# Kernel tuning notes

Hardware: AMD Instinct MI355X
Metric: run time of the kernel (lower is better)

The kernel has to match this reference:

```python
import jax, jax.numpy as jnp
import numpy as np

B, L, DIN, DQK = 16, 1024, 512, 128
NL, NC = 2, 2  # number of 'learnable' heads, number of 'cnn_projection' heads


def _conv1d(x_bcl, w, b):
    # x: [B, C_in, L], w: [C_out, C_in, 3], 'same' padding (kernel 3 -> pad 1)
    y = jax.lax.conv_general_dilated(x_bcl, w, (1,), [(1, 1)],
                                     dimension_numbers=('NCH', 'OIH', 'NCH'))
    return y + b[None, :, None]


def _attend(q, k, v, scale):
    # q,k,v: [H, B, L, D]; scale: [H]
    inv = 1.0 / jnp.sqrt(jnp.asarray(q.shape[-1], q.dtype))
    att = jax.nn.softmax(jnp.einsum('hbld,hbmd->hblm', q, k) * inv, axis=-1)
    out = scale[:, None, None, None] * jnp.einsum('hblm,hbmd->hbld', att, v)
    return out, att


def setup_inputs() -> dict:
    rk = jax.random.key(0)
    ks = jax.random.split(rk, 24)
    s = 0.02
    d = {}
    d['query'] = jax.random.normal(ks[0], (B, L, DIN), jnp.float32)
    d['key']   = jax.random.normal(ks[1], (B, L, DIN), jnp.float32)
    d['value'] = jax.random.normal(ks[2], (B, L, DIN), jnp.float32)
    # learnable (KQVProduct) heads: Linear dim_in -> dim_qk, stored as [in,out]
    d['lw_q'] = jax.random.normal(ks[3], (NL, DIN, DQK), jnp.float32) * s
    d['lb_q'] = jnp.zeros((NL, DQK), jnp.float32)
    d['lw_k'] = jax.random.normal(ks[4], (NL, DIN, DQK), jnp.float32) * s
    d['lb_k'] = jnp.zeros((NL, DQK), jnp.float32)
    d['lw_v'] = jax.random.normal(ks[5], (NL, DIN, DQK), jnp.float32) * s
    d['lb_v'] = jnp.zeros((NL, DQK), jnp.float32)
    d['lscale'] = jnp.ones((NL,), jnp.float32)
    # cnn_projection (KQVPCNN) heads: Conv1d(dim_in, dim_qk, k=3, pad=1)
    d['cw_q'] = jax.random.normal(ks[6], (NC, DQK, DIN, 3), jnp.float32) * s
    d['cb_q'] = jnp.zeros((NC, DQK), jnp.float32)
    d['cw_k'] = jax.random.normal(ks[7], (NC, DQK, DIN, 3), jnp.float32) * s
    d['cb_k'] = jnp.zeros((NC, DQK), jnp.float32)
    d['cw_v'] = jax.random.normal(ks[8], (NC, DQK, DIN, 3), jnp.float32) * s
    d['cb_v'] = jnp.zeros((NC, DQK), jnp.float32)
    d['cscale'] = jnp.ones((NC,), jnp.float32)
    # final projection: Linear((NL+NC)*dim_qk -> dim_in)
    d['proj_w'] = jax.random.normal(ks[9], ((NL + NC) * DQK, DIN), jnp.float32) * s
    d['proj_b'] = jnp.zeros((DIN,), jnp.float32)
    return d


def reference(query, key, value,
              lw_q, lb_q, lw_k, lb_k, lw_v, lb_v, lscale,
              cw_q, cb_q, cw_k, cb_k, cw_v, cb_v, cscale,
              proj_w, proj_b):
    # --- learnable heads (batched over head axis) ---
    lq = jnp.einsum('bld,hdk->hblk', query, lw_q) + lb_q[:, None, None, :]
    lk = jnp.einsum('bld,hdk->hblk', key,   lw_k) + lb_k[:, None, None, :]
    lv = jnp.einsum('bld,hdk->hblk', value, lw_v) + lb_v[:, None, None, :]
    lout, latt = _attend(lq, lk, lv, lscale)
    # --- cnn_projection heads ---
    qt = jnp.swapaxes(query, 1, 2)  # [B, DIN, L]
    kt = jnp.swapaxes(key, 1, 2)
    vt = jnp.swapaxes(value, 1, 2)
    cq = jnp.swapaxes(jax.vmap(lambda w, b: _conv1d(qt, w, b))(cw_q, cb_q), 2, 3)
    ck = jnp.swapaxes(jax.vmap(lambda w, b: _conv1d(kt, w, b))(cw_k, cb_k), 2, 3)
    cv = jnp.swapaxes(jax.vmap(lambda w, b: _conv1d(vt, w, b))(cw_v, cb_v), 2, 3)
    cout, catt = _attend(cq, ck, cv, cscale)  # [NC, B, L, DQK]
    # --- concat heads + final projection ---
    cat = jnp.concatenate([lout[0], lout[1], cout[0], cout[1]], axis=-1)  # [B,L,4*DQK]
    out = cat @ proj_w + proj_b
    return (out, latt[0], latt[1], catt[0], catt[1])
```

## Files before the change

kernel.cpp:

```cpp
#include <hip/hip_runtime.h>


using bf16_t = __bf16;
using bf16x8 = __attribute__((ext_vector_type(8))) __bf16;
using bf16x4 = __attribute__((ext_vector_type(4))) __bf16;
using f32x4  = __attribute__((ext_vector_type(4))) float;

#define NB   16
#define SL   1024
#define DIN  512
#define DQK  128
#define NH   4

#define BK 32

constexpr size_t XPAD_ROWS  = (size_t)NB * (SL + 2);
constexpr size_t XPAD_PER   = XPAD_ROWS * DIN;
constexpr size_t XPAD_ELEMS = 3 * XPAD_PER;
constexpr size_t WT_ELEMS   = (size_t)3 * NH * 3 * DQK * DIN;
constexpr size_t PWT_ELEMS  = (size_t)DIN * DIN;
constexpr size_t BIAS_ELEMS = (size_t)3 * NH * DQK;
constexpr size_t QH_ELEMS   = (size_t)NH * NB * SL * DQK;
constexpr size_t ATTB_ELEMS = (size_t)NH * NB * SL * SL;
constexpr size_t CAT_ELEMS  = (size_t)NB * SL * (NH * DQK);

#define INV_SQRT_DK 0.08838834764831845f

__device__ __forceinline__ void load_lds_16B(const void* g, void* l) {
  __builtin_amdgcn_global_load_lds((const __attribute__((address_space(1))) void*)g,
                                   (__attribute__((address_space(3))) void*)l, 16, 0, 0);
}

__device__ __forceinline__ void gemm_core(const bf16_t* __restrict__ Ab, int lda,
                                          const bf16_t* __restrict__ Bb, int ldb,
                                          int K, f32x4 acc[4][4],
                                          bf16_t* lgA, bf16_t* lgB) {
  const int tid  = threadIdx.x;
  const int wave = tid >> 6;
  const int lane = tid & 63;
  const int quad = lane >> 4;
  const int l16  = lane & 15;
  const int wr   = wave >> 1;
  const int wc   = wave & 1;
  const int lrow = lane >> 2;
  const int lcol = (lane & 3) << 3;

  for (int k0 = 0; k0 < K; k0 += BK) {
    __syncthreads();
#pragma unroll
    for (int c = 0; c < 2; ++c) {
      const int chunk = wave * 2 + c;
      const int r = chunk * 16 + lrow;
      load_lds_16B(Ab + (size_t)r * lda + k0 + lcol, lgA + chunk * 512);
      load_lds_16B(Bb + (size_t)r * ldb + k0 + lcol, lgB + chunk * 512);
    }
    __syncthreads();
    bf16x8 af[4], bfr[4];
#pragma unroll
    for (int i = 0; i < 4; ++i)
      af[i] = *(const bf16x8*)(lgA + (wr * 64 + i * 16 + l16) * BK + quad * 8);
#pragma unroll
    for (int i = 0; i < 4; ++i)
      bfr[i] = *(const bf16x8*)(lgB + (wc * 64 + i * 16 + l16) * BK + quad * 8);
#pragma unroll
    for (int mi = 0; mi < 4; ++mi)
#pragma unroll
      for (int ni = 0; ni < 4; ++ni)
        acc[mi][ni] = __builtin_amdgcn_mfma_f32_16x16x32_bf16(af[mi], bfr[ni],
                                                              acc[mi][ni], 0, 0, 0);
  }
}

#define GEMM_PROLOGUE()                                    \
  __shared__ __align__(16) bf16_t lgA[128 * BK];           \
  __shared__ __align__(16) bf16_t lgB[128 * BK];           \
  f32x4 acc[4][4];                                         \
  {                                                        \
    f32x4 z = {0.f, 0.f, 0.f, 0.f};                        \
    _Pragma("unroll") for (int i = 0; i < 4; ++i)          \
      _Pragma("unroll") for (int j = 0; j < 4; ++j)        \
        acc[i][j] = z;                                     \
  }

#define EPILOGUE_VARS()                                    \
  const int wave = threadIdx.x >> 6;                       \
  const int lane = threadIdx.x & 63;                       \
  const int quad = lane >> 4;                              \
  const int l16  = lane & 15;                              \
  const int wr   = wave >> 1;                              \
  const int wc   = wave & 1;


__global__ void cast_pad_kernel(const float* __restrict__ q,
                                const float* __restrict__ k,
                                const float* __restrict__ v,
                                bf16_t* __restrict__ xpad) {
  size_t i = (size_t)blockIdx.x * blockDim.x + threadIdx.x;
  if (i >= XPAD_ELEMS / 8) return;
  int    s    = (int)(i / (XPAD_PER / 8));
  size_t r    = i % (XPAD_PER / 8);
  size_t rowg = r >> 6;
  int    c0   = (int)(r & 63) * 8;
  size_t b    = rowg / (SL + 2);
  int    row  = (int)(rowg % (SL + 2));
  const float* src = (s == 0) ? q : ((s == 1) ? k : v);
  bf16x8 o;
  if (row == 0 || row == SL + 1) {
#pragma unroll
    for (int j = 0; j < 8; ++j) o[j] = (bf16_t)0.f;
  } else {
    const float* p = src + ((b * SL) + row - 1) * DIN + c0;
    const float4 f0 = ((const float4*)p)[0];
    const float4 f1 = ((const float4*)p)[1];
    o[0] = (bf16_t)f0.x; o[1] = (bf16_t)f0.y; o[2] = (bf16_t)f0.z; o[3] = (bf16_t)f0.w;
    o[4] = (bf16_t)f1.x; o[5] = (bf16_t)f1.y; o[6] = (bf16_t)f1.z; o[7] = (bf16_t)f1.w;
  }
  *(bf16x8*)(xpad + i * 8) = o;
}

__global__ void prep_w_kernel(const float* __restrict__ lw_q, const float* __restrict__ lw_k,
                              const float* __restrict__ lw_v, const float* __restrict__ lb_q,
                              const float* __restrict__ lb_k, const float* __restrict__ lb_v,
                              const float* __restrict__ cw_q, const float* __restrict__ cw_k,
                              const float* __restrict__ cw_v, const float* __restrict__ cb_q,
                              const float* __restrict__ cb_k, const float* __restrict__ cb_v,
                              const float* __restrict__ proj_w,
                              bf16_t* __restrict__ Wt, float* __restrict__ bias,
                              bf16_t* __restrict__ pwt) {
  size_t i = (size_t)blockIdx.x * blockDim.x + threadIdx.x;
  if (i < WT_ELEMS) {
    int kk = (int)(i % DIN);
    int n  = (int)((i / DIN) % DQK);
    int t  = (int)((i / ((size_t)DIN * DQK)) % 3);
    int h  = (int)((i / ((size_t)DIN * DQK * 3)) % NH);
    int s  = (int)(i / ((size_t)DIN * DQK * 3 * NH));
    const float* lw = (s == 0) ? lw_q : ((s == 1) ? lw_k : lw_v);
    const float* cw = (s == 0) ? cw_q : ((s == 1) ? cw_k : cw_v);
    float val;
    if (h < 2) val = (t == 1) ? lw[((size_t)h * DIN + kk) * DQK + n] : 0.f;
    else       val = cw[(((size_t)(h - 2) * DQK + n) * DIN + kk) * 3 + t];
    Wt[i] = (bf16_t)val;
  } else if (i < WT_ELEMS + PWT_ELEMS) {
    size_t j = i - WT_ELEMS;
    int n = (int)(j / DIN), kk = (int)(j % DIN);
    pwt[j] = (bf16_t)proj_w[(size_t)kk * DIN + n];
  } else if (i < WT_ELEMS + PWT_ELEMS + BIAS_ELEMS) {
    size_t j = i - WT_ELEMS - PWT_ELEMS;
    int s = (int)(j / (NH * DQK));
    int h = (int)((j / DQK) % NH);
    int n = (int)(j % DQK);
    const float* lb = (s == 0) ? lb_q : ((s == 1) ? lb_k : lb_v);
    const float* cb = (s == 0) ? cb_q : ((s == 1) ? cb_k : cb_v);
    bias[j] = (h < 2) ? lb[h * DQK + n] : cb[(h - 2) * DQK + n];
  }
}

__global__ __launch_bounds__(256, 2) void proj_kernel(
    const bf16_t* __restrict__ xpad, const bf16_t* __restrict__ Wt,
    const float* __restrict__ bias,
    bf16_t* __restrict__ Qh, bf16_t* __restrict__ Kh, bf16_t* __restrict__ Vt) {
  GEMM_PROLOGUE();
  const int mt = blockIdx.x;
  const int z  = blockIdx.z;
  const int s  = z >> 2, h = z & 3;
  const int b  = mt >> 3;
  const int l0 = (mt & 7) << 7;

  const bf16_t* Xs = xpad + (size_t)s * XPAD_PER;
  const int t0 = (h < 2) ? 1 : 0;
  const int t1 = (h < 2) ? 1 : 2;
  for (int t = t0; t <= t1; ++t) {
    const bf16_t* Ab = Xs + ((size_t)b * (SL + 2) + l0 + t) * DIN;
    const bf16_t* Bb = Wt + (((size_t)(s * NH + h) * 3 + t) * DQK) * DIN;
    gemm_core(Ab, DIN, Bb, DIN, DIN, acc, lgA, lgB);
  }

  EPILOGUE_VARS();
  const float* bs = bias + (s * NH + h) * DQK;
  if (s < 2) {
    bf16_t* outp = ((s == 0) ? Qh : Kh) + ((size_t)h * NB + b) * SL * DQK
                 + (size_t)l0 * DQK;
#pragma unroll
    for (int mi = 0; mi < 4; ++mi)
#pragma unroll
      for (int ni = 0; ni < 4; ++ni)
#pragma unroll
        for (int r = 0; r < 4; ++r) {
          int row = wr * 64 + mi * 16 + quad * 4 + r;
          int col = wc * 64 + ni * 16 + l16;
          outp[(size_t)row * DQK + col] = (bf16_t)(acc[mi][ni][r] + bs[col]);
        }
  } else {
    bf16_t* outv = Vt + ((size_t)h * NB + b) * DQK * SL;
#pragma unroll
    for (int mi = 0; mi < 4; ++mi)
#pragma unroll
      for (int ni = 0; ni < 4; ++ni)
#pragma unroll
        for (int r = 0; r < 4; ++r) {
          int row = wr * 64 + mi * 16 + quad * 4 + r;
          int col = wc * 64 + ni * 16 + l16;
          outv[(size_t)col * SL + l0 + row] = (bf16_t)(acc[mi][ni][r] + bs[col]);
        }
  }
}

__global__ __launch_bounds__(256, 2) void sgemm_kernel(
    const bf16_t* __restrict__ Qh, const bf16_t* __restrict__ Kh,
    float* __restrict__ att) {
  GEMM_PROLOGUE();
  const int mt = blockIdx.x;
  const int nt = blockIdx.y;
  const int hb = blockIdx.z;
  const bf16_t* Ab = Qh + (size_t)hb * SL * DQK + (size_t)mt * 128 * DQK;
  const bf16_t* Bb = Kh + (size_t)hb * SL * DQK + (size_t)nt * 128 * DQK;
  gemm_core(Ab, DQK, Bb, DQK, DQK, acc, lgA, lgB);

  EPILOGUE_VARS();
  float* outp = att + (size_t)hb * SL * SL;
#pragma unroll
  for (int mi = 0; mi < 4; ++mi)
#pragma unroll
    for (int ni = 0; ni < 4; ++ni)
#pragma unroll
      for (int r = 0; r < 4; ++r) {
        int row = mt * 128 + wr * 64 + mi * 16 + quad * 4 + r;
        int col = nt * 128 + wc * 64 + ni * 16 + l16;
        outp[(size_t)row * SL + col] = acc[mi][ni][r] * INV_SQRT_DK;
      }
}

__global__ __launch_bounds__(256) void softmax_kernel(float* __restrict__ att,
                                                      bf16_t* __restrict__ attb) {
  const size_t row = blockIdx.x;
  float* p = att + row * SL;
  const int tid = threadIdx.x;
  float4 v = ((const float4*)p)[tid];

  float m = fmaxf(fmaxf(v.x, v.y), fmaxf(v.z, v.w));
#pragma unroll
  for (int off = 32; off; off >>= 1) m = fmaxf(m, __shfl_xor(m, off, 64));
  __shared__ float redm[4];
  __shared__ float reds[4];
  const int wv = tid >> 6, ln = tid & 63;
  if (ln == 0) redm[wv] = m;
  __syncthreads();
  m = fmaxf(fmaxf(redm[0], redm[1]), fmaxf(redm[2], redm[3]));

  float e0 = __expf(v.x - m), e1 = __expf(v.y - m);
  float e2 = __expf(v.z - m), e3 = __expf(v.w - m);
  float s = e0 + e1 + e2 + e3;
#pragma unroll
  for (int off = 32; off; off >>= 1) s += __shfl_xor(s, off, 64);
  if (ln == 0) reds[wv] = s;
  __syncthreads();
  s = reds[0] + reds[1] + reds[2] + reds[3];
  const float inv = 1.0f / s;

  float4 o = {e0 * inv, e1 * inv, e2 * inv, e3 * inv};
  ((float4*)p)[tid] = o;
  bf16x4 ob = {(bf16_t)o.x, (bf16_t)o.y, (bf16_t)o.z, (bf16_t)o.w};
  *(bf16x4*)(attb + row * SL + tid * 4) = ob;
}

__global__ __launch_bounds__(256, 2) void av_kernel(
    const bf16_t* __restrict__ attb, const bf16_t* __restrict__ Vt,
    const float* __restrict__ lscale, const float* __restrict__ cscale,
    bf16_t* __restrict__ cat) {
  GEMM_PROLOGUE();
  const int mt = blockIdx.x;
  const int hb = blockIdx.z;
  const int h = hb >> 4, b = hb & 15;
  const bf16_t* Ab = attb + (size_t)hb * SL * SL + (size_t)mt * 128 * SL;
  const bf16_t* Bb = Vt + (size_t)hb * DQK * SL;
  gemm_core(Ab, SL, Bb, SL, SL, acc, lgA, lgB);

  EPILOGUE_VARS();
  const float sc = (h < 2) ? lscale[h] : cscale[h - 2];
  bf16_t* outp = cat + (size_t)b * SL * (NH * DQK) + (size_t)(mt * 128) * (NH * DQK)
               + h * DQK;
#pragma unroll
  for (int mi = 0; mi < 4; ++mi)
#pragma unroll
    for (int ni = 0; ni < 4; ++ni)
#pragma unroll
      for (int r = 0; r < 4; ++r) {
        int row = wr * 64 + mi * 16 + quad * 4 + r;
        int col = wc * 64 + ni * 16 + l16;
        outp[(size_t)row * (NH * DQK) + col] = (bf16_t)(acc[mi][ni][r] * sc);
      }
}

__global__ __launch_bounds__(256, 2) void final_kernel(
    const bf16_t* __restrict__ cat, const bf16_t* __restrict__ pwt,
    const float* __restrict__ pb, float* __restrict__ outp) {
  GEMM_PROLOGUE();
  const int mt = blockIdx.x;
  const int nt = blockIdx.y;
  const bf16_t* Ab = cat + (size_t)mt * 128 * DIN;
  const bf16_t* Bb = pwt + (size_t)nt * 128 * DIN;
  gemm_core(Ab, DIN, Bb, DIN, DIN, acc, lgA, lgB);

  EPILOGUE_VARS();
#pragma unroll
  for (int mi = 0; mi < 4; ++mi)
#pragma unroll
    for (int ni = 0; ni < 4; ++ni)
#pragma unroll
      for (int r = 0; r < 4; ++r) {
        int row = mt * 128 + wr * 64 + mi * 16 + quad * 4 + r;
        int col = nt * 128 + wc * 64 + ni * 16 + l16;
        outp[(size_t)row * DIN + col] = acc[mi][ni][r] + pb[nt * 128 + col];
      }
}


extern "C" void kernel_launch(void* const* d_in, const int* in_sizes, int n_in,
                              void* d_out, int out_size, void* d_ws, size_t ws_size,
                              hipStream_t stream) {
  const float* q      = (const float*)d_in[0];
  const float* k      = (const float*)d_in[1];
  const float* v      = (const float*)d_in[2];
  const float* lw_q   = (const float*)d_in[3];
  const float* lb_q   = (const float*)d_in[4];
  const float* lw_k   = (const float*)d_in[5];
  const float* lb_k   = (const float*)d_in[6];
  const float* lw_v   = (const float*)d_in[7];
  const float* lb_v   = (const float*)d_in[8];
  const float* lscale = (const float*)d_in[9];
  const float* cw_q   = (const float*)d_in[10];
  const float* cb_q   = (const float*)d_in[11];
  const float* cw_k   = (const float*)d_in[12];
  const float* cb_k   = (const float*)d_in[13];
  const float* cw_v   = (const float*)d_in[14];
  const float* cb_v   = (const float*)d_in[15];
  const float* cscale = (const float*)d_in[16];
  const float* proj_w = (const float*)d_in[17];
  const float* proj_b = (const float*)d_in[18];

  char* ws = (char*)d_ws;
  size_t off = 0;
  bf16_t* xpad = (bf16_t*)(ws + off); off += XPAD_ELEMS * 2;
  bf16_t* Wt   = (bf16_t*)(ws + off); off += WT_ELEMS * 2;
  float*  bias = (float*) (ws + off); off += BIAS_ELEMS * 4;
  bf16_t* pwt  = (bf16_t*)(ws + off); off += PWT_ELEMS * 2;
  bf16_t* Qh   = (bf16_t*)(ws + off); off += QH_ELEMS * 2;
  bf16_t* Kh   = (bf16_t*)(ws + off); off += QH_ELEMS * 2;
  bf16_t* Vt   = (bf16_t*)(ws + off); off += QH_ELEMS * 2;
  bf16_t* attb = (bf16_t*)(ws + off); off += ATTB_ELEMS * 2;
  bf16_t* cat  = (bf16_t*)(ws + off); off += CAT_ELEMS * 2;

  float* outp = (float*)d_out;
  float* att  = outp + (size_t)NB * SL * DIN;

  {
    int nblk = (int)((XPAD_ELEMS / 8 + 255) / 256);
    cast_pad_kernel<<<nblk, 256, 0, stream>>>(q, k, v, xpad);
  }
  {
    size_t tot = WT_ELEMS + PWT_ELEMS + BIAS_ELEMS;
    int nblk = (int)((tot + 255) / 256);
    prep_w_kernel<<<nblk, 256, 0, stream>>>(lw_q, lw_k, lw_v, lb_q, lb_k, lb_v,
                                            cw_q, cw_k, cw_v, cb_q, cb_k, cb_v,
                                            proj_w, Wt, bias, pwt);
  }
  proj_kernel<<<dim3(128, 1, 12), 256, 0, stream>>>(xpad, Wt, bias, Qh, Kh, Vt);
  sgemm_kernel<<<dim3(8, 8, 64), 256, 0, stream>>>(Qh, Kh, att);
  softmax_kernel<<<NH * NB * SL, 256, 0, stream>>>(att, attb);
  av_kernel<<<dim3(8, 1, 64), 256, 0, stream>>>(attb, Vt, lscale, cscale, cat);
  final_kernel<<<dim3(128, 4, 1), 256, 0, stream>>>(cat, pwt, proj_b, outp);
}
```

Baseline: 695.6 us.

## Fuse softmax into score GEMM partial stats and AV kernel normalization

Removes the standalone softmax kernel and the bf16 attention buffer. The score GEMM now also emits per-tile row max and sum partials, and the AV kernel merges them, normalizes the fp32 scores in place while streaming them, and feeds bf16 probabilities to LDS for the MFMA. This cuts one full read and write pass over the large attention matrix plus the bf16 copy. In exchange, the AV A-operand is now loaded synchronously in registers rather than with async LDS loads. The proj_kernel also flips the head order per z index, likely to balance tap-count work across blocks.

```diff
diff --git a/kernel.cpp b/kernel.cpp
--- a/kernel.cpp
+++ b/kernel.cpp
@@ -21,7 +21,7 @@
 constexpr size_t PWT_ELEMS  = (size_t)DIN * DIN;
 constexpr size_t BIAS_ELEMS = (size_t)3 * NH * DQK;
 constexpr size_t QH_ELEMS   = (size_t)NH * NB * SL * DQK;
-constexpr size_t ATTB_ELEMS = (size_t)NH * NB * SL * SL;
+constexpr size_t PART_ELEMS = (size_t)NH * NB * 8 * SL;
 constexpr size_t CAT_ELEMS  = (size_t)NB * SL * (NH * DQK);
 
 #define INV_SQRT_DK 0.08838834764831845f
@@ -162,7 +162,7 @@
   GEMM_PROLOGUE();
   const int mt = blockIdx.x;
   const int z  = blockIdx.z;
-  const int s  = z >> 2, h = z & 3;
+  const int s  = z >> 2, h = (z & 3) ^ 2;
   const int b  = mt >> 3;
   const int l0 = (mt & 7) << 7;
 
@@ -207,7 +207,7 @@
 
 __global__ __launch_bounds__(256, 2) void sgemm_kernel(
     const bf16_t* __restrict__ Qh, const bf16_t* __restrict__ Kh,
-    float* __restrict__ att) {
+    float* __restrict__ att, float2* __restrict__ partials) {
   GEMM_PROLOGUE();
   const int mt = blockIdx.x;
   const int nt = blockIdx.y;
@@ -217,6 +217,15 @@
   gemm_core(Ab, DQK, Bb, DQK, DQK, acc, lgA, lgB);
 
   EPILOGUE_VARS();
+  const int tid = threadIdx.x;
+#pragma unroll
+  for (int mi = 0; mi < 4; ++mi)
+#pragma unroll
+    for (int ni = 0; ni < 4; ++ni)
+#pragma unroll
+      for (int r = 0; r < 4; ++r)
+        acc[mi][ni][r] *= INV_SQRT_DK;
+
   float* outp = att + (size_t)hb * SL * SL;
 #pragma unroll
   for (int mi = 0; mi < 4; ++mi)
@@ -226,56 +235,156 @@
       for (int r = 0; r < 4; ++r) {
         int row = mt * 128 + wr * 64 + mi * 16 + quad * 4 + r;
         int col = nt * 128 + wc * 64 + ni * 16 + l16;
-        outp[(size_t)row * SL + col] = acc[mi][ni][r] * INV_SQRT_DK;
+        outp[(size_t)row * SL + col] = acc[mi][ni][r];
       }
-}
-
-__global__ __launch_bounds__(256) void softmax_kernel(float* __restrict__ att,
-                                                      bf16_t* __restrict__ attb) {
-  const size_t row = blockIdx.x;
-  float* p = att + row * SL;
-  const int tid = threadIdx.x;
-  float4 v = ((const float4*)p)[tid];
-
-  float m = fmaxf(fmaxf(v.x, v.y), fmaxf(v.z, v.w));
-#pragma unroll
-  for (int off = 32; off; off >>= 1) m = fmaxf(m, __shfl_xor(m, off, 64));
-  __shared__ float redm[4];
-  __shared__ float reds[4];
-  const int wv = tid >> 6, ln = tid & 63;
-  if (ln == 0) redm[wv] = m;
+
   __syncthreads();
-  m = fmaxf(fmaxf(redm[0], redm[1]), fmaxf(redm[2], redm[3]));
-
-  float e0 = __expf(v.x - m), e1 = __expf(v.y - m);
-  float e2 = __expf(v.z - m), e3 = __expf(v.w - m);
-  float s = e0 + e1 + e2 + e3;
-#pragma unroll
-  for (int off = 32; off; off >>= 1) s += __shfl_xor(s, off, 64);
-  if (ln == 0) reds[wv] = s;
+  float* smM = (float*)lgA;
+  float* smS = smM + 256;
+#pragma unroll
+  for (int mi = 0; mi < 4; ++mi)
+#pragma unroll
+    for (int r = 0; r < 4; ++r) {
+      float m = acc[mi][0][r];
+#pragma unroll
+      for (int ni = 1; ni < 4; ++ni) m = fmaxf(m, acc[mi][ni][r]);
+      m = fmaxf(m, __shfl_xor(m, 1, 64));
+      m = fmaxf(m, __shfl_xor(m, 2, 64));
+      m = fmaxf(m, __shfl_xor(m, 4, 64));
+      m = fmaxf(m, __shfl_xor(m, 8, 64));
+      float s = 0.f;
+#pragma unroll
+      for (int ni = 0; ni < 4; ++ni) s += __expf(acc[mi][ni][r] - m);
+      s += __shfl_xor(s, 1, 64);
+      s += __shfl_xor(s, 2, 64);
+      s += __shfl_xor(s, 4, 64);
+      s += __shfl_xor(s, 8, 64);
+      if (l16 == 0) {
+        int row = wr * 64 + mi * 16 + quad * 4 + r;
+        smM[row * 2 + wc] = m;
+        smS[row * 2 + wc] = s;
+      }
+    }
   __syncthreads();
-  s = reds[0] + reds[1] + reds[2] + reds[3];
-  const float inv = 1.0f / s;
-
-  float4 o = {e0 * inv, e1 * inv, e2 * inv, e3 * inv};
-  ((float4*)p)[tid] = o;
-  bf16x4 ob = {(bf16_t)o.x, (bf16_t)o.y, (bf16_t)o.z, (bf16_t)o.w};
-  *(bf16x4*)(attb + row * SL + tid * 4) = ob;
+  if (tid < 128) {
+    float m0 = smM[tid * 2], m1 = smM[tid * 2 + 1];
+    float s0 = smS[tid * 2], s1 = smS[tid * 2 + 1];
+    float m = fmaxf(m0, m1);
+    float s = s0 * __expf(m0 - m) + s1 * __expf(m1 - m);
+    partials[((size_t)hb * 8 + nt) * SL + (size_t)mt * 128 + tid] =
+        make_float2(m, s);
+  }
 }
 
 __global__ __launch_bounds__(256, 2) void av_kernel(
-    const bf16_t* __restrict__ attb, const bf16_t* __restrict__ Vt,
+    float* __restrict__ att, const float2* __restrict__ partials,
+    const bf16_t* __restrict__ Vt,
     const float* __restrict__ lscale, const float* __restrict__ cscale,
     bf16_t* __restrict__ cat) {
-  GEMM_PROLOGUE();
+  __shared__ __align__(16) bf16_t lgA[128 * BK];
+  __shared__ __align__(16) bf16_t lgB[128 * BK];
+  __shared__ float rowM[128];
+  __shared__ float rowInv[128];
+  f32x4 acc[4][4];
+  {
+    f32x4 z = {0.f, 0.f, 0.f, 0.f};
+#pragma unroll
+    for (int i = 0; i < 4; ++i)
+#pragma unroll
+      for (int j = 0; j < 4; ++j) acc[i][j] = z;
+  }
   const int mt = blockIdx.x;
   const int hb = blockIdx.z;
   const int h = hb >> 4, b = hb & 15;
-  const bf16_t* Ab = attb + (size_t)hb * SL * SL + (size_t)mt * 128 * SL;
+  const int tid = threadIdx.x;
+
+  if (tid < 128) {
+    const size_t g = (size_t)mt * 128 + tid;
+    float2 t[8];
+    float m = -__builtin_inff();
+#pragma unroll
+    for (int nt = 0; nt < 8; ++nt) {
+      t[nt] = partials[((size_t)hb * 8 + nt) * SL + g];
+      m = fmaxf(m, t[nt].x);
+    }
+    float s = 0.f;
+#pragma unroll
+    for (int nt = 0; nt < 8; ++nt) s += t[nt].y * __expf(t[nt].x - m);
+    rowM[tid] = m;
+    rowInv[tid] = 1.0f / s;
+  }
+  __syncthreads();
+
+  const int arow = tid >> 1;
+  const int acol = (tid & 1) * 16;
+  const float rm = rowM[arow];
+  const float ri = rowInv[arow];
+  float* Sp = att + (size_t)hb * SL * SL + ((size_t)mt * 128 + arow) * SL + acol;
+
+  const int wave = tid >> 6;
+  const int lane = tid & 63;
+  const int quad = lane >> 4;
+  const int l16  = lane & 15;
+  const int wr   = wave >> 1;
+  const int wc   = wave & 1;
+  const int lrow = lane >> 2;
+  const int lcol = (lane & 3) << 3;
   const bf16_t* Bb = Vt + (size_t)hb * DQK * SL;
-  gemm_core(Ab, SL, Bb, SL, SL, acc, lgA, lgB);
-
-  EPILOGUE_VARS();
+
+  float4 f0 = ((const float4*)Sp)[0];
+  float4 f1 = ((const float4*)Sp)[1];
+  float4 f2 = ((const float4*)Sp)[2];
+  float4 f3 = ((const float4*)Sp)[3];
+
+  for (int k0 = 0; k0 < SL; k0 += BK) {
+    __syncthreads();
+    float4 p0, p1, p2, p3;
+    p0.x = __expf(f0.x - rm) * ri; p0.y = __expf(f0.y - rm) * ri;
+    p0.z = __expf(f0.z - rm) * ri; p0.w = __expf(f0.w - rm) * ri;
+    p1.x = __expf(f1.x - rm) * ri; p1.y = __expf(f1.y - rm) * ri;
+    p1.z = __expf(f1.z - rm) * ri; p1.w = __expf(f1.w - rm) * ri;
+    p2.x = __expf(f2.x - rm) * ri; p2.y = __expf(f2.y - rm) * ri;
+    p2.z = __expf(f2.z - rm) * ri; p2.w = __expf(f2.w - rm) * ri;
+    p3.x = __expf(f3.x - rm) * ri; p3.y = __expf(f3.y - rm) * ri;
+    p3.z = __expf(f3.z - rm) * ri; p3.w = __expf(f3.w - rm) * ri;
+    ((float4*)(Sp + k0))[0] = p0;
+    ((float4*)(Sp + k0))[1] = p1;
+    ((float4*)(Sp + k0))[2] = p2;
+    ((float4*)(Sp + k0))[3] = p3;
+    bf16x8 o0 = {(bf16_t)p0.x, (bf16_t)p0.y, (bf16_t)p0.z, (bf16_t)p0.w,
+                 (bf16_t)p1.x, (bf16_t)p1.y, (bf16_t)p1.z, (bf16_t)p1.w};
+    bf16x8 o1 = {(bf16_t)p2.x, (bf16_t)p2.y, (bf16_t)p2.z, (bf16_t)p2.w,
+                 (bf16_t)p3.x, (bf16_t)p3.y, (bf16_t)p3.z, (bf16_t)p3.w};
+    *(bf16x8*)(lgA + arow * BK + acol)     = o0;
+    *(bf16x8*)(lgA + arow * BK + acol + 8) = o1;
+    if (k0 + BK < SL) {
+      f0 = ((const float4*)(Sp + k0 + BK))[0];
+      f1 = ((const float4*)(Sp + k0 + BK))[1];
+      f2 = ((const float4*)(Sp + k0 + BK))[2];
+      f3 = ((const float4*)(Sp + k0 + BK))[3];
+    }
+#pragma unroll
+    for (int c = 0; c < 2; ++c) {
+      const int chunk = wave * 2 + c;
+      const int r = chunk * 16 + lrow;
+      load_lds_16B(Bb + (size_t)r * SL + k0 + lcol, lgB + chunk * 512);
+    }
+    __syncthreads();
+    bf16x8 af[4], bfr[4];
+#pragma unroll
+    for (int i = 0; i < 4; ++i)
+      af[i] = *(const bf16x8*)(lgA + (wr * 64 + i * 16 + l16) * BK + quad * 8);
+#pragma unroll
+    for (int i = 0; i < 4; ++i)
+      bfr[i] = *(const bf16x8*)(lgB + (wc * 64 + i * 16 + l16) * BK + quad * 8);
+#pragma unroll
+    for (int mi = 0; mi < 4; ++mi)
+#pragma unroll
+      for (int ni = 0; ni < 4; ++ni)
+        acc[mi][ni] = __builtin_amdgcn_mfma_f32_16x16x32_bf16(af[mi], bfr[ni],
+                                                              acc[mi][ni], 0, 0, 0);
+  }
+
   const float sc = (h < 2) ? lscale[h] : cscale[h - 2];
   bf16_t* outp = cat + (size_t)b * SL * (NH * DQK) + (size_t)(mt * 128) * (NH * DQK)
                + h * DQK;
@@ -340,15 +449,15 @@
 
   char* ws = (char*)d_ws;
   size_t off = 0;
-  bf16_t* xpad = (bf16_t*)(ws + off); off += XPAD_ELEMS * 2;
-  bf16_t* Wt   = (bf16_t*)(ws + off); off += WT_ELEMS * 2;
-  float*  bias = (float*) (ws + off); off += BIAS_ELEMS * 4;
-  bf16_t* pwt  = (bf16_t*)(ws + off); off += PWT_ELEMS * 2;
-  bf16_t* Qh   = (bf16_t*)(ws + off); off += QH_ELEMS * 2;
-  bf16_t* Kh   = (bf16_t*)(ws + off); off += QH_ELEMS * 2;
-  bf16_t* Vt   = (bf16_t*)(ws + off); off += QH_ELEMS * 2;
-  bf16_t* attb = (bf16_t*)(ws + off); off += ATTB_ELEMS * 2;
-  bf16_t* cat  = (bf16_t*)(ws + off); off += CAT_ELEMS * 2;
+  bf16_t* xpad  = (bf16_t*)(ws + off); off += XPAD_ELEMS * 2;
+  bf16_t* Wt    = (bf16_t*)(ws + off); off += WT_ELEMS * 2;
+  float*  bias  = (float*) (ws + off); off += BIAS_ELEMS * 4;
+  bf16_t* pwt   = (bf16_t*)(ws + off); off += PWT_ELEMS * 2;
+  bf16_t* Qh    = (bf16_t*)(ws + off); off += QH_ELEMS * 2;
+  bf16_t* Kh    = (bf16_t*)(ws + off); off += QH_ELEMS * 2;
+  bf16_t* Vt    = (bf16_t*)(ws + off); off += QH_ELEMS * 2;
+  float2* parts = (float2*)(ws + off); off += PART_ELEMS * 8;
+  bf16_t* cat   = (bf16_t*)(ws + off); off += CAT_ELEMS * 2;
 
   float* outp = (float*)d_out;
   float* att  = outp + (size_t)NB * SL * DIN;
@@ -365,8 +474,7 @@
                                             proj_w, Wt, bias, pwt);
   }
   proj_kernel<<<dim3(128, 1, 12), 256, 0, stream>>>(xpad, Wt, bias, Qh, Kh, Vt);
-  sgemm_kernel<<<dim3(8, 8, 64), 256, 0, stream>>>(Qh, Kh, att);
-  softmax_kernel<<<NH * NB * SL, 256, 0, stream>>>(att, attb);
-  av_kernel<<<dim3(8, 1, 64), 256, 0, stream>>>(attb, Vt, lscale, cscale, cat);
+  sgemm_kernel<<<dim3(8, 8, 64), 256, 0, stream>>>(Qh, Kh, att, parts);
+  av_kernel<<<dim3(8, 1, 64), 256, 0, stream>>>(att, parts, Vt, lscale, cscale, cat);
   final_kernel<<<dim3(128, 4, 1), 256, 0, stream>>>(cat, pwt, proj_b, outp);
 }
```

Result: faster. 680.9 us (-2.1%).

## Fuse QK^T, softmax and AV into one two-pass flash-style attention kernel

Applied to the files above, without the earlier changes.

Replaces the separate score GEMM, softmax and AV GEMM kernels with one fused kernel. Each 64-row query tile runs a first pass over K to get the row max and sum online, then a second pass that recomputes the scores, writes the normalized fp32 probabilities directly and multiplies them by V from LDS. This removes the fp32 score round trip through memory, the bf16 probability buffer and two launches, at the cost of computing QK^T twice. It also reorders the proj head mapping and swizzles the block index across heads and batches.

```diff
diff --git a/kernel.cpp b/kernel.cpp
--- a/kernel.cpp
+++ b/kernel.cpp
@@ -3,7 +3,6 @@
 
 using bf16_t = __bf16;
 using bf16x8 = __attribute__((ext_vector_type(8))) __bf16;
-using bf16x4 = __attribute__((ext_vector_type(4))) __bf16;
 using f32x4  = __attribute__((ext_vector_type(4))) float;
 
 #define NB   16
@@ -21,7 +20,6 @@
 constexpr size_t PWT_ELEMS  = (size_t)DIN * DIN;
 constexpr size_t BIAS_ELEMS = (size_t)3 * NH * DQK;
 constexpr size_t QH_ELEMS   = (size_t)NH * NB * SL * DQK;
-constexpr size_t ATTB_ELEMS = (size_t)NH * NB * SL * SL;
 constexpr size_t CAT_ELEMS  = (size_t)NB * SL * (NH * DQK);
 
 #define INV_SQRT_DK 0.08838834764831845f
@@ -162,7 +160,7 @@
   GEMM_PROLOGUE();
   const int mt = blockIdx.x;
   const int z  = blockIdx.z;
-  const int s  = z >> 2, h = z & 3;
+  const int s  = z >> 2, h = (z & 3) ^ 2;
   const int b  = mt >> 3;
   const int l0 = (mt & 7) << 7;
 
@@ -205,90 +203,153 @@
   }
 }
 
-__global__ __launch_bounds__(256, 2) void sgemm_kernel(
+__global__ __launch_bounds__(256, 3) void fattn_kernel(
     const bf16_t* __restrict__ Qh, const bf16_t* __restrict__ Kh,
-    float* __restrict__ att) {
-  GEMM_PROLOGUE();
-  const int mt = blockIdx.x;
-  const int nt = blockIdx.y;
-  const int hb = blockIdx.z;
-  const bf16_t* Ab = Qh + (size_t)hb * SL * DQK + (size_t)mt * 128 * DQK;
-  const bf16_t* Bb = Kh + (size_t)hb * SL * DQK + (size_t)nt * 128 * DQK;
-  gemm_core(Ab, DQK, Bb, DQK, DQK, acc, lgA, lgB);
-
-  EPILOGUE_VARS();
-  float* outp = att + (size_t)hb * SL * SL;
-#pragma unroll
-  for (int mi = 0; mi < 4; ++mi)
-#pragma unroll
-    for (int ni = 0; ni < 4; ++ni)
-#pragma unroll
-      for (int r = 0; r < 4; ++r) {
-        int row = mt * 128 + wr * 64 + mi * 16 + quad * 4 + r;
-        int col = nt * 128 + wc * 64 + ni * 16 + l16;
-        outp[(size_t)row * SL + col] = acc[mi][ni][r] * INV_SQRT_DK;
+    const bf16_t* __restrict__ Vt,
+    const float* __restrict__ lscale, const float* __restrict__ cscale,
+    float* __restrict__ att, bf16_t* __restrict__ cat) {
+  __shared__ __align__(16) bf16_t stKV[128 * 128];
+  __shared__ __align__(16) bf16_t eL[64 * 128];
+
+  const int flat = blockIdx.x;
+  const int hb   = (flat & 7) * 8 + ((flat >> 3) & 7);
+  const int mt   = flat >> 6;
+  const int h = hb >> 4, b = hb & 15;
+
+  const int tid  = threadIdx.x;
+  const int wave = tid >> 6;
+  const int lane = tid & 63;
+  const int quad = lane >> 4;
+  const int l16  = lane & 15;
+  const int row_l = wave * 16 + l16;
+
+  const bf16_t* Qb = Qh + (size_t)hb * SL * DQK + (size_t)(mt * 64) * DQK;
+  const bf16_t* Kb = Kh + (size_t)hb * SL * DQK;
+  const bf16_t* Vb = Vt + (size_t)hb * DQK * SL;
+  float* attp = att + (size_t)hb * SL * SL;
+
+  bf16x8 af_q[4];
+#pragma unroll
+  for (int kk = 0; kk < 4; ++kk)
+    af_q[kk] = *(const bf16x8*)(Qb + (size_t)row_l * DQK + kk * 32 + quad * 8);
+
+#define STAGE_SWZ(srcbase, srs)                                               \
+  {                                                                           \
+    _Pragma("unroll") for (int i = 0; i < 8; ++i) {                           \
+      const int slot = (wave * 8 + i) * 64 + lane;                            \
+      const int n = slot >> 4, kc = slot & 15;                                \
+      load_lds_16B((srcbase) + (size_t)n * (srs) + ((kc ^ (n & 15)) << 3),    \
+                   stKV + (size_t)(wave * 8 + i) * 512);                      \
+    }                                                                         \
+  }
+
+#define S_MFMA(aS)                                                            \
+  {                                                                           \
+    _Pragma("unroll") for (int kk = 0; kk < 4; ++kk)                          \
+      _Pragma("unroll") for (int ni = 0; ni < 8; ++ni) {                      \
+        const int n = ni * 16 + l16;                                          \
+        const bf16x8 bf = *(const bf16x8*)((const char*)stKV + n * 256 +      \
+                              ((kk * 64 + quad * 16) ^ ((n & 15) << 4)));     \
+        aS[ni] = __builtin_amdgcn_mfma_f32_16x16x32_bf16(af_q[kk], bf,        \
+                                                         aS[ni], 0, 0, 0);    \
+      }                                                                       \
+  }
+
+  float M[4], Ssum[4];
+#pragma unroll
+  for (int r = 0; r < 4; ++r) { M[r] = -3.0e38f; Ssum[r] = 0.f; }
+
+  for (int nt = 0; nt < 8; ++nt) {
+    __syncthreads();
+    STAGE_SWZ(Kb + (size_t)nt * 128 * DQK, DQK);
+    __syncthreads();
+    f32x4 aS[8];
+#pragma unroll
+    for (int ni = 0; ni < 8; ++ni) aS[ni] = f32x4{0.f, 0.f, 0.f, 0.f};
+    S_MFMA(aS);
+#pragma unroll
+    for (int r = 0; r < 4; ++r) {
+      float v[8];
+#pragma unroll
+      for (int ni = 0; ni < 8; ++ni) v[ni] = aS[ni][r] * INV_SQRT_DK;
+      float m = fmaxf(fmaxf(fmaxf(v[0], v[1]), fmaxf(v[2], v[3])),
+                      fmaxf(fmaxf(v[4], v[5]), fmaxf(v[6], v[7])));
+      m = fmaxf(m, __shfl_xor(m, 1, 64));
+      m = fmaxf(m, __shfl_xor(m, 2, 64));
+      m = fmaxf(m, __shfl_xor(m, 4, 64));
+      m = fmaxf(m, __shfl_xor(m, 8, 64));
+      float s = 0.f;
+#pragma unroll
+      for (int ni = 0; ni < 8; ++ni) s += __expf(v[ni] - m);
+      s += __shfl_xor(s, 1, 64);
+      s += __shfl_xor(s, 2, 64);
+      s += __shfl_xor(s, 4, 64);
+      s += __shfl_xor(s, 8, 64);
+      const float Mn = fmaxf(M[r], m);
+      Ssum[r] = Ssum[r] * __expf(M[r] - Mn) + s * __expf(m - Mn);
+      M[r] = Mn;
+    }
+  }
+  float cinv[4];
+#pragma unroll
+  for (int r = 0; r < 4; ++r) cinv[r] = 1.0f / Ssum[r];
+
+  f32x4 accO[8];
+#pragma unroll
+  for (int ni = 0; ni < 8; ++ni) accO[ni] = f32x4{0.f, 0.f, 0.f, 0.f};
+
+  for (int nt = 0; nt < 8; ++nt) {
+    __syncthreads();
+    STAGE_SWZ(Kb + (size_t)nt * 128 * DQK, DQK);
+    __syncthreads();
+    f32x4 aS[8];
+#pragma unroll
+    for (int ni = 0; ni < 8; ++ni) aS[ni] = f32x4{0.f, 0.f, 0.f, 0.f};
+    S_MFMA(aS);
+#pragma unroll
+    for (int r = 0; r < 4; ++r) {
+      const int rowl  = wave * 16 + quad * 4 + r;
+      const int row_g = mt * 64 + rowl;
+      float* rp = attp + (size_t)row_g * SL + nt * 128 + l16;
+#pragma unroll
+      for (int ni = 0; ni < 8; ++ni) {
+        const float p = __expf(aS[ni][r] * INV_SQRT_DK - M[r]) * cinv[r];
+        rp[ni * 16] = p;
+        *(bf16_t*)((char*)eL + rowl * 256 +
+                   (((ni * 16 + l16) * 2) ^ ((rowl & 15) << 4))) = (bf16_t)p;
       }
-}
-
-__global__ __launch_bounds__(256) void softmax_kernel(float* __restrict__ att,
-                                                      bf16_t* __restrict__ attb) {
-  const size_t row = blockIdx.x;
-  float* p = att + row * SL;
-  const int tid = threadIdx.x;
-  float4 v = ((const float4*)p)[tid];
-
-  float m = fmaxf(fmaxf(v.x, v.y), fmaxf(v.z, v.w));
-#pragma unroll
-  for (int off = 32; off; off >>= 1) m = fmaxf(m, __shfl_xor(m, off, 64));
-  __shared__ float redm[4];
-  __shared__ float reds[4];
-  const int wv = tid >> 6, ln = tid & 63;
-  if (ln == 0) redm[wv] = m;
-  __syncthreads();
-  m = fmaxf(fmaxf(redm[0], redm[1]), fmaxf(redm[2], redm[3]));
-
-  float e0 = __expf(v.x - m), e1 = __expf(v.y - m);
-  float e2 = __expf(v.z - m), e3 = __expf(v.w - m);
-  float s = e0 + e1 + e2 + e3;
-#pragma unroll
-  for (int off = 32; off; off >>= 1) s += __shfl_xor(s, off, 64);
-  if (ln == 0) reds[wv] = s;
-  __syncthreads();
-  s = reds[0] + reds[1] + reds[2] + reds[3];
-  const float inv = 1.0f / s;
-
-  float4 o = {e0 * inv, e1 * inv, e2 * inv, e3 * inv};
-  ((float4*)p)[tid] = o;
-  bf16x4 ob = {(bf16_t)o.x, (bf16_t)o.y, (bf16_t)o.z, (bf16_t)o.w};
-  *(bf16x4*)(attb + row * SL + tid * 4) = ob;
-}
-
-__global__ __launch_bounds__(256, 2) void av_kernel(
-    const bf16_t* __restrict__ attb, const bf16_t* __restrict__ Vt,
-    const float* __restrict__ lscale, const float* __restrict__ cscale,
-    bf16_t* __restrict__ cat) {
-  GEMM_PROLOGUE();
-  const int mt = blockIdx.x;
-  const int hb = blockIdx.z;
-  const int h = hb >> 4, b = hb & 15;
-  const bf16_t* Ab = attb + (size_t)hb * SL * SL + (size_t)mt * 128 * SL;
-  const bf16_t* Bb = Vt + (size_t)hb * DQK * SL;
-  gemm_core(Ab, SL, Bb, SL, SL, acc, lgA, lgB);
-
-  EPILOGUE_VARS();
+    }
+    __syncthreads();
+    STAGE_SWZ(Vb + (size_t)nt * 128, SL);
+    __syncthreads();
+#pragma unroll
+    for (int kk = 0; kk < 4; ++kk) {
+      const bf16x8 ap = *(const bf16x8*)((const char*)eL + row_l * 256 +
+                            ((kk * 64 + quad * 16) ^ ((row_l & 15) << 4)));
+#pragma unroll
+      for (int ni = 0; ni < 8; ++ni) {
+        const int d = ni * 16 + l16;
+        const bf16x8 bv = *(const bf16x8*)((const char*)stKV + d * 256 +
+                              ((kk * 64 + quad * 16) ^ ((d & 15) << 4)));
+        accO[ni] = __builtin_amdgcn_mfma_f32_16x16x32_bf16(ap, bv, accO[ni],
+                                                           0, 0, 0);
+      }
+    }
+  }
+
   const float sc = (h < 2) ? lscale[h] : cscale[h - 2];
-  bf16_t* outp = cat + (size_t)b * SL * (NH * DQK) + (size_t)(mt * 128) * (NH * DQK)
-               + h * DQK;
-#pragma unroll
-  for (int mi = 0; mi < 4; ++mi)
-#pragma unroll
-    for (int ni = 0; ni < 4; ++ni)
-#pragma unroll
-      for (int r = 0; r < 4; ++r) {
-        int row = wr * 64 + mi * 16 + quad * 4 + r;
-        int col = wc * 64 + ni * 16 + l16;
-        outp[(size_t)row * (NH * DQK) + col] = (bf16_t)(acc[mi][ni][r] * sc);
-      }
+  bf16_t* outp = cat + (size_t)b * SL * (NH * DQK) + h * DQK;
+#pragma unroll
+  for (int r = 0; r < 4; ++r) {
+    const int row_g = mt * 64 + wave * 16 + quad * 4 + r;
+#pragma unroll
+    for (int ni = 0; ni < 8; ++ni) {
+      const int col = ni * 16 + l16;
+      outp[(size_t)row_g * (NH * DQK) + col] = (bf16_t)(accO[ni][r] * sc);
+    }
+  }
+#undef STAGE_SWZ
+#undef S_MFMA
 }
 
 __global__ __launch_bounds__(256, 2) void final_kernel(
@@ -347,7 +408,6 @@
   bf16_t* Qh   = (bf16_t*)(ws + off); off += QH_ELEMS * 2;
   bf16_t* Kh   = (bf16_t*)(ws + off); off += QH_ELEMS * 2;
   bf16_t* Vt   = (bf16_t*)(ws + off); off += QH_ELEMS * 2;
-  bf16_t* attb = (bf16_t*)(ws + off); off += ATTB_ELEMS * 2;
   bf16_t* cat  = (bf16_t*)(ws + off); off += CAT_ELEMS * 2;
 
   float* outp = (float*)d_out;
@@ -365,8 +425,7 @@
                                             proj_w, Wt, bias, pwt);
   }
   proj_kernel<<<dim3(128, 1, 12), 256, 0, stream>>>(xpad, Wt, bias, Qh, Kh, Vt);
-  sgemm_kernel<<<dim3(8, 8, 64), 256, 0, stream>>>(Qh, Kh, att);
-  softmax_kernel<<<NH * NB * SL, 256, 0, stream>>>(att, attb);
-  av_kernel<<<dim3(8, 1, 64), 256, 0, stream>>>(attb, Vt, lscale, cscale, cat);
+  fattn_kernel<<<dim3(1024, 1, 1), 256, 0, stream>>>(Qh, Kh, Vt, lscale, cscale,
+                                                     att, cat);
   final_kernel<<<dim3(128, 4, 1), 256, 0, stream>>>(cat, pwt, proj_b, outp);
 }
```

Measured after the change: 730.4 us. +5.0%, slower.
